# Kernel optimization log

Measured on AMD Instinct MI355X. Metric: run time of the kernel, lower is better.

Reference implementation:

```python
import jax, jax.numpy as jnp
import numpy as np

BS, C, H, W = 4, 128, 64, 64  # input_dim=128
INNER = 64


def setup_inputs() -> dict:
    key = jax.random.key(0)
    ks = jax.random.split(key, 9)
    s_in = 1.0 / np.sqrt(C)
    s_inner = 1.0 / np.sqrt(INNER)
    return {
        "inpt": jax.random.normal(ks[0], (BS, C, H, W), dtype=jnp.float32),
        "Wq": jax.random.normal(ks[1], (INNER, C), dtype=jnp.float32) * s_in,
        "bq": jax.random.normal(ks[2], (INNER,), dtype=jnp.float32) * 0.01,
        "Wk": jax.random.normal(ks[3], (INNER, C), dtype=jnp.float32) * s_in,
        "bk": jax.random.normal(ks[4], (INNER,), dtype=jnp.float32) * 0.01,
        "Wv": jax.random.normal(ks[5], (INNER, C), dtype=jnp.float32) * s_in,
        "bv": jax.random.normal(ks[6], (INNER,), dtype=jnp.float32) * 0.01,
        "Wo": jax.random.normal(ks[7], (C, INNER), dtype=jnp.float32) * s_inner,
        "bo": jax.random.normal(ks[8], (C,), dtype=jnp.float32) * 0.01,
    }


def reference(inpt, Wq, bq, Wk, bk, Wv, bv, Wo, bo):
    bs, c, h, w = inpt.shape
    L = h * w
    # [bs, C, H, W] -> [bs, L, C] (tokens = spatial positions)
    x = inpt.reshape(bs, c, L).transpose(0, 2, 1)
    q = jnp.einsum('blc,dc->bld', x, Wq) + bq  # [bs, L, INNER]
    k = jnp.einsum('blc,dc->bld', x, Wk) + bk
    v = jnp.einsum('blc,dc->bld', x, Wv) + bv
    # torch code divides by np.round(sqrt(d), 2); for d=64 this is exactly 8.0
    scale = jnp.float32(np.round(np.sqrt(q.shape[-1]), 2))
    scores = jnp.einsum('bld,bmd->blm', q, k) / scale  # [bs, L, L] score matrix
    factors = jax.nn.softmax(scores, axis=-1)
    ctx = jnp.einsum('blm,bmd->bld', factors, v)  # [bs, L, INNER]
    out = jnp.einsum('bld,cd->blc', ctx, Wo) + bo  # [bs, L, C]
    out = out.transpose(0, 2, 1).reshape(bs, c, h, w)
    return inpt + out
```

## Files before the change

kernel.cpp:

```cpp
#include <hip/hip_runtime.h>
#include <hip/hip_bf16.h>

typedef __bf16 bf16x8 __attribute__((ext_vector_type(8)));
typedef __bf16 bf16x4 __attribute__((ext_vector_type(4)));
typedef short  s16x4  __attribute__((ext_vector_type(4)));
typedef float  f32x4  __attribute__((ext_vector_type(4)));

#define MFMA32(a, b, c) __builtin_amdgcn_mfma_f32_16x16x32_bf16((a), (b), (c), 0, 0, 0)
#define MFMA16K(a, b, c) __builtin_amdgcn_mfma_f32_16x16x16bf16_1k((a), (b), (c), 0, 0, 0)

#if __has_builtin(__builtin_amdgcn_exp2f)
#define EXP2F(x) __builtin_amdgcn_exp2f(x)
#else
#define EXP2F(x) __expf(0.6931471805599453f * (x))
#endif

#define GL16(G, L)                                                            \
    __builtin_amdgcn_global_load_lds(                                         \
        (const __attribute__((address_space(1))) void*)(G),                   \
        (__attribute__((address_space(3))) void*)(L), 16, 0, 0)

#define SPLIT 4
#define QSCALE 0.18033688011112042f
#define BBOUND 12.0f


__global__ __launch_bounds__(256) void qkv_kernel(
    const float* __restrict__ inpt,
    const float* __restrict__ Wq, const float* __restrict__ bq,
    const float* __restrict__ Wk, const float* __restrict__ bk,
    const float* __restrict__ Wv, const float* __restrict__ bv,
    __bf16* __restrict__ Qws, __bf16* __restrict__ Kws, __bf16* __restrict__ VTws)
{
    __shared__ __align__(16) __bf16 xT[16 * 140];
    __shared__ __align__(16) __bf16 os[16 * 144];
    const int bid = blockIdx.x;
    const int b   = bid >> 8;
    const int l0  = (bid & 255) << 4;
    const int t   = threadIdx.x;

    {
        const int c = t >> 1, half = t & 1;
        const float* xin = inpt + ((size_t)(b * 128 + c)) * 4096 + l0 + half * 8;
        float4 v0 = *(const float4*)xin;
        float4 v1 = *(const float4*)(xin + 4);
        const int tok0 = half * 8;
        xT[(tok0 + 0) * 140 + c] = (__bf16)v0.x;
        xT[(tok0 + 1) * 140 + c] = (__bf16)v0.y;
        xT[(tok0 + 2) * 140 + c] = (__bf16)v0.z;
        xT[(tok0 + 3) * 140 + c] = (__bf16)v0.w;
        xT[(tok0 + 4) * 140 + c] = (__bf16)v1.x;
        xT[(tok0 + 5) * 140 + c] = (__bf16)v1.y;
        xT[(tok0 + 6) * 140 + c] = (__bf16)v1.z;
        xT[(tok0 + 7) * 140 + c] = (__bf16)v1.w;
    }
    __syncthreads();

    const int w    = t >> 6;
    const int lane = t & 63;
    const int quad = lane >> 4;
    const int l15  = lane & 15;

    f32x4 acc[3];
    #pragma unroll
    for (int j = 0; j < 3; ++j)
        #pragma unroll
        for (int r = 0; r < 4; ++r) acc[j][r] = 0.f;

    #pragma unroll
    for (int ks = 0; ks < 4; ++ks) {
        bf16x8 af = *(const bf16x8*)&xT[l15 * 140 + ks * 32 + quad * 8];
        #pragma unroll
        for (int j = 0; j < 3; ++j) {
            const int wn   = w * 3 + j;
            const int msel = wn >> 2;
            const float* W = (msel == 0) ? Wq : ((msel == 1) ? Wk : Wv);
            const float* Wp = W + ((wn & 3) * 16 + l15) * 128 + ks * 32 + quad * 8;
            float4 wa = *(const float4*)Wp;
            float4 wb = *(const float4*)(Wp + 4);
            bf16x8 bf;
            bf[0] = (__bf16)wa.x; bf[1] = (__bf16)wa.y;
            bf[2] = (__bf16)wa.z; bf[3] = (__bf16)wa.w;
            bf[4] = (__bf16)wb.x; bf[5] = (__bf16)wb.y;
            bf[6] = (__bf16)wb.z; bf[7] = (__bf16)wb.w;
            acc[j] = MFMA32(af, bf, acc[j]);
        }
    }

    #pragma unroll
    for (int j = 0; j < 3; ++j) {
        const int wn   = w * 3 + j;
        const int msel = wn >> 2;
        const int o0   = (wn & 3) * 16;
        const float* bb = (msel == 0) ? bq : ((msel == 1) ? bk : bv);
        float bias = bb[o0 + l15];
        if (msel < 2) {
            const float scl = (msel == 0) ? QSCALE : 1.0f;
            const int oc = wn * 16 + l15;
            #pragma unroll
            for (int r = 0; r < 4; ++r)
                os[(quad * 4 + r) * 144 + oc] = (__bf16)((acc[j][r] + bias) * scl);
        } else {
            const int d  = o0 + l15;
            const int kt = l0 >> 6;
            const int kc = (l0 >> 4) & 3;
            bf16x4 v;
            #pragma unroll
            for (int r = 0; r < 4; ++r) v[r] = (__bf16)(acc[j][r] + bias);
            *(bf16x4*)(VTws + (size_t)b * 262144 + kt * 4096
                       + d * 64 + quad * 16 + kc * 4) = v;
        }
    }
    __syncthreads();

    {
        const int tok = t >> 4, c = t & 15;
        bf16x8 v = *(const bf16x8*)&os[tok * 144 + c * 8];
        __bf16* dst = (c < 8)
            ? Qws + ((size_t)(b * 4096 + l0 + tok)) * 64 + c * 8
            : Kws + ((size_t)(b * 4096 + l0 + tok)) * 64 + (c - 8) * 8;
        *(bf16x8*)dst = v;
    }
}

__global__ __launch_bounds__(256, 4) void attn_kernel(
    const __bf16* __restrict__ Qws, const __bf16* __restrict__ Kws,
    const __bf16* __restrict__ VTws,
    float* __restrict__ Ops, float* __restrict__ Lws)
{
    __shared__ __align__(16) __bf16 sbuf[2][8192];

    const int bid   = blockIdx.x;
    const int split = bid >> 8;
    const int qt    = bid & 255;
    const int b  = qt >> 6;
    const int l0 = (qt & 63) << 6;
    const int t    = threadIdx.x;
    const int w    = t >> 6;
    const int lane = t & 63;
    const int quad = lane >> 4;
    const int l15  = lane & 15;

    const __bf16* qptr = Qws + ((size_t)(b * 4096 + l0 + w * 16 + l15)) * 64 + quad * 8;
    bf16x8 qf0 = *(const bf16x8*)qptr;
    bf16x8 qf1 = *(const bf16x8*)(qptr + 32);

    f32x4 cfr[4];
    #pragma unroll
    for (int mt = 0; mt < 4; ++mt)
        #pragma unroll
        for (int r = 0; r < 4; ++r) cfr[mt][r] = 0.f;
    float l_run = 0.f;

    int koff[8], voff[8];
    #pragma unroll
    for (int nt = 0; nt < 4; ++nt) {
        const int key = nt * 16 + l15;
        const int kx  = key & 7;
        koff[nt * 2 + 0] = (key * 8 + (quad ^ kx)) * 8;
        koff[nt * 2 + 1] = (key * 8 + ((quad + 4) ^ kx)) * 8;
    }
    #pragma unroll
    for (int mt = 0; mt < 4; ++mt) {
        const int d = mt * 16 + l15;
        #pragma unroll
        for (int kc8 = 0; kc8 < 2; ++kc8)
            voff[kc8 * 4 + mt] = 4096 + d * 64 + (((2 * quad + kc8) ^ (d & 7)) * 8);
    }

    const uint4* Kg = (const uint4*)(Kws + ((size_t)b << 18));
    const uint4* Vg = (const uint4*)(VTws + ((size_t)b << 18));
    const int rw = t >> 3, cw = (t & 7) ^ ((t >> 3) & 7);
    const uint4* kp = Kg + rw * 8 + cw + split * 8192;
    const uint4* vp = Vg + rw * 8 + cw + split * 8192;

    union B4 { bf16x4 h; s16x4 s; };
    union V8 { bf16x8 v; s16x4 q[2]; };

    auto stage = [&](__bf16* Bb) {
        GL16(kp,       Bb +        w * 512);
        GL16(kp + 256, Bb + 2048 + w * 512);
        GL16(vp,       Bb + 4096 + w * 512);
        GL16(vp + 256, Bb + 6144 + w * 512);
        kp += 512; vp += 512;
    };

    auto tile_step = [&](const __bf16* __restrict__ B) {
        B4 pk[4];
        float ps[4];
        #pragma unroll
        for (int nt = 0; nt < 4; ++nt) {
            bf16x8 kf0 = *(const bf16x8*)&B[koff[nt * 2 + 0]];
            bf16x8 kf1 = *(const bf16x8*)&B[koff[nt * 2 + 1]];
            f32x4 a = {-BBOUND, -BBOUND, -BBOUND, -BBOUND};
            a = MFMA32(kf0, qf0, a);
            a = MFMA32(kf1, qf1, a);
            float p0 = EXP2F(a[0]), p1 = EXP2F(a[1]);
            float p2 = EXP2F(a[2]), p3 = EXP2F(a[3]);
            pk[nt].h[0] = (__bf16)p0; pk[nt].h[1] = (__bf16)p1;
            pk[nt].h[2] = (__bf16)p2; pk[nt].h[3] = (__bf16)p3;
            ps[nt] = (p0 + p1) + (p2 + p3);
        }
        float psum = (ps[0] + ps[1]) + (ps[2] + ps[3]);
        psum += __shfl_xor(psum, 16);
        psum += __shfl_xor(psum, 32);
        l_run += psum;

        #pragma unroll
        for (int kc8 = 0; kc8 < 2; ++kc8) {
            #pragma unroll
            for (int mt = 0; mt < 4; ++mt) {
                V8 vv;
                vv.v = *(const bf16x8*)&B[voff[kc8 * 4 + mt]];
                cfr[mt] = MFMA16K(vv.q[0], pk[2 * kc8 + 0].s, cfr[mt]);
                cfr[mt] = MFMA16K(vv.q[1], pk[2 * kc8 + 1].s, cfr[mt]);
            }
        }
    };

    stage(sbuf[0]);

    __bf16* B0 = sbuf[0];
    __bf16* B1 = sbuf[1];
    for (int kt2 = 0; kt2 < 8; ++kt2) {
        __syncthreads();
        stage(B1);
        tile_step(B0);
        __syncthreads();
        if (kt2 < 7) stage(B0);
        tile_step(B1);
    }

    const int l   = l0 + w * 16 + l15;
    const int row = (split * 4 + b) * 4096 + l;
    float* obase = Ops + (size_t)row * 64;
    #pragma unroll
    for (int mt = 0; mt < 4; ++mt)
        *(f32x4*)(obase + mt * 16 + quad * 4) = cfr[mt];
    if (quad == 0) Lws[row] = l_run;
}

__global__ __launch_bounds__(256) void outproj_kernel(
    const float* __restrict__ inpt,
    const float* __restrict__ Ops, const float* __restrict__ Lws,
    const float* __restrict__ Wo, const float* __restrict__ bo,
    float* __restrict__ out)
{
    __shared__ __align__(16) __bf16 cx[16 * 72];
    const int bid = blockIdx.x;
    const int b   = bid >> 8;
    const int l0  = (bid & 255) << 4;
    const int t   = threadIdx.x;

    {
        const int token = t >> 4, d4 = (t & 15) << 2;
        const int rowb  = b * 4096 + l0 + token;
        float denom = 0.f;
        #pragma unroll
        for (int s = 0; s < SPLIT; ++s) denom += Lws[s * 16384 + rowb];
        const float inv = 1.f / denom;
        float ax = 0.f, ay = 0.f, az = 0.f, aw = 0.f;
        #pragma unroll
        for (int s = 0; s < SPLIT; ++s) {
            const float4 v = *(const float4*)(Ops + ((size_t)(s * 16384 + rowb)) * 64 + d4);
            ax += v.x; ay += v.y; az += v.z; aw += v.w;
        }
        bf16x4 pv;
        pv[0] = (__bf16)(ax * inv); pv[1] = (__bf16)(ay * inv);
        pv[2] = (__bf16)(az * inv); pv[3] = (__bf16)(aw * inv);
        *(bf16x4*)&cx[token * 72 + d4] = pv;
    }
    __syncthreads();

    const int w    = t >> 6;
    const int lane = t & 63;
    const int quad = lane >> 4;
    const int l15  = lane & 15;

    f32x4 acc[2];
    #pragma unroll
    for (int mi = 0; mi < 2; ++mi)
        #pragma unroll
        for (int r = 0; r < 4; ++r) acc[mi][r] = 0.f;

    #pragma unroll
    for (int ks = 0; ks < 2; ++ks) {
        bf16x8 bfrag = *(const bf16x8*)&cx[l15 * 72 + ks * 32 + quad * 8];
        #pragma unroll
        for (int mi = 0; mi < 2; ++mi) {
            const int crow = (w * 2 + mi) * 16 + l15;
            const float* Wp = Wo + crow * 64 + ks * 32 + quad * 8;
            float4 wa = *(const float4*)Wp;
            float4 wb = *(const float4*)(Wp + 4);
            bf16x8 afrag;
            afrag[0] = (__bf16)wa.x; afrag[1] = (__bf16)wa.y;
            afrag[2] = (__bf16)wa.z; afrag[3] = (__bf16)wa.w;
            afrag[4] = (__bf16)wb.x; afrag[5] = (__bf16)wb.y;
            afrag[6] = (__bf16)wb.z; afrag[7] = (__bf16)wb.w;
            acc[mi] = MFMA32(afrag, bfrag, acc[mi]);
        }
    }

    #pragma unroll
    for (int mi = 0; mi < 2; ++mi) {
        #pragma unroll
        for (int r = 0; r < 4; ++r) {
            const int c = (w * 2 + mi) * 16 + quad * 4 + r;
            const size_t addr = ((size_t)(b * 128 + c)) * 4096 + l0 + l15;
            out[addr] = inpt[addr] + bo[c] + acc[mi][r];
        }
    }
}

extern "C" void kernel_launch(void* const* d_in, const int* in_sizes, int n_in,
                              void* d_out, int out_size, void* d_ws, size_t ws_size,
                              hipStream_t stream)
{
    const float* inpt = (const float*)d_in[0];
    const float* Wq   = (const float*)d_in[1];
    const float* bq   = (const float*)d_in[2];
    const float* Wk   = (const float*)d_in[3];
    const float* bk   = (const float*)d_in[4];
    const float* Wv   = (const float*)d_in[5];
    const float* bv   = (const float*)d_in[6];
    const float* Wo   = (const float*)d_in[7];
    const float* bo   = (const float*)d_in[8];
    float* out = (float*)d_out;

    char* ws = (char*)d_ws;
    const size_t MB = (size_t)1 << 20;
    __bf16* Qws  = (__bf16*)(ws + 0 * MB);
    __bf16* Kws  = (__bf16*)(ws + 2 * MB);
    __bf16* VTws = (__bf16*)(ws + 4 * MB);
    float*  Ops  = (float*)(ws + 6 * MB);
    float*  Lws  = (float*)(ws + 23 * MB);

    qkv_kernel<<<1024, 256, 0, stream>>>(inpt, Wq, bq, Wk, bk, Wv, bv, Qws, Kws, VTws);
    attn_kernel<<<SPLIT * 256, 256, 0, stream>>>(Qws, Kws, VTws, Ops, Lws);
    outproj_kernel<<<1024, 256, 0, stream>>>(inpt, Ops, Lws, Wo, bo, out);
}
```

Baseline: 125.9 us.

## Double query rows per wave, split keys eightfold, store partial outputs in bf16

Each wave now handles two 16-row query tiles and reuses every K/V fragment loaded from LDS for both, which halves LDS traffic per unit of MFMA work. The key dimension is split 8 ways instead of 4, so each block walks 512 keys and the grid stays at 1024 blocks. Partial context outputs are written as bf16 instead of fp32, which shrinks the workspace write and the later reduction read. The trade-offs are more registers per thread (two accumulator sets), which may limit occupancy, twice as many partials to combine, and extra rounding from storing unnormalised partials in bf16.

```diff
diff --git a/kernel.cpp b/kernel.cpp
--- a/kernel.cpp
+++ b/kernel.cpp
@@ -20,7 +20,7 @@
         (const __attribute__((address_space(1))) void*)(G),                   \
         (__attribute__((address_space(3))) void*)(L), 16, 0, 0)
 
-#define SPLIT 4
+#define SPLIT 8
 #define QSCALE 0.18033688011112042f
 #define BBOUND 12.0f
 
@@ -126,31 +126,38 @@
 __global__ __launch_bounds__(256, 4) void attn_kernel(
     const __bf16* __restrict__ Qws, const __bf16* __restrict__ Kws,
     const __bf16* __restrict__ VTws,
-    float* __restrict__ Ops, float* __restrict__ Lws)
+    __bf16* __restrict__ Ops, float* __restrict__ Lws)
 {
     __shared__ __align__(16) __bf16 sbuf[2][8192];
 
     const int bid   = blockIdx.x;
-    const int split = bid >> 8;
-    const int qt    = bid & 255;
-    const int b  = qt >> 6;
-    const int l0 = (qt & 63) << 6;
+    const int split = bid >> 7;
+    const int rest  = bid & 127;
+    const int b   = rest >> 5;
+    const int l0  = (rest & 31) << 7;
     const int t    = threadIdx.x;
     const int w    = t >> 6;
     const int lane = t & 63;
     const int quad = lane >> 4;
     const int l15  = lane & 15;
 
-    const __bf16* qptr = Qws + ((size_t)(b * 4096 + l0 + w * 16 + l15)) * 64 + quad * 8;
-    bf16x8 qf0 = *(const bf16x8*)qptr;
-    bf16x8 qf1 = *(const bf16x8*)(qptr + 32);
-
-    f32x4 cfr[4];
-    #pragma unroll
-    for (int mt = 0; mt < 4; ++mt)
-        #pragma unroll
-        for (int r = 0; r < 4; ++r) cfr[mt][r] = 0.f;
-    float l_run = 0.f;
+    bf16x8 qf[2][2];
+    #pragma unroll
+    for (int u = 0; u < 2; ++u) {
+        const __bf16* qptr = Qws
+            + ((size_t)(b * 4096 + l0 + w * 32 + u * 16 + l15)) * 64 + quad * 8;
+        qf[u][0] = *(const bf16x8*)qptr;
+        qf[u][1] = *(const bf16x8*)(qptr + 32);
+    }
+
+    f32x4 cfr[2][4];
+    #pragma unroll
+    for (int u = 0; u < 2; ++u)
+        #pragma unroll
+        for (int mt = 0; mt < 4; ++mt)
+            #pragma unroll
+            for (int r = 0; r < 4; ++r) cfr[u][mt][r] = 0.f;
+    float l_run[2] = {0.f, 0.f};
 
     int koff[8], voff[8];
     #pragma unroll
@@ -171,8 +178,8 @@
     const uint4* Kg = (const uint4*)(Kws + ((size_t)b << 18));
     const uint4* Vg = (const uint4*)(VTws + ((size_t)b << 18));
     const int rw = t >> 3, cw = (t & 7) ^ ((t >> 3) & 7);
-    const uint4* kp = Kg + rw * 8 + cw + split * 8192;
-    const uint4* vp = Vg + rw * 8 + cw + split * 8192;
+    const uint4* kp = Kg + rw * 8 + cw + split * 4096;
+    const uint4* vp = Vg + rw * 8 + cw + split * 4096;
 
     union B4 { bf16x4 h; s16x4 s; };
     union V8 { bf16x8 v; s16x4 q[2]; };
@@ -186,25 +193,31 @@
     };
 
     auto tile_step = [&](const __bf16* __restrict__ B) {
-        B4 pk[4];
-        float ps[4];
+        B4 pk[2][4];
+        float ps[2][4];
         #pragma unroll
         for (int nt = 0; nt < 4; ++nt) {
             bf16x8 kf0 = *(const bf16x8*)&B[koff[nt * 2 + 0]];
             bf16x8 kf1 = *(const bf16x8*)&B[koff[nt * 2 + 1]];
-            f32x4 a = {-BBOUND, -BBOUND, -BBOUND, -BBOUND};
-            a = MFMA32(kf0, qf0, a);
-            a = MFMA32(kf1, qf1, a);
-            float p0 = EXP2F(a[0]), p1 = EXP2F(a[1]);
-            float p2 = EXP2F(a[2]), p3 = EXP2F(a[3]);
-            pk[nt].h[0] = (__bf16)p0; pk[nt].h[1] = (__bf16)p1;
-            pk[nt].h[2] = (__bf16)p2; pk[nt].h[3] = (__bf16)p3;
-            ps[nt] = (p0 + p1) + (p2 + p3);
-        }
-        float psum = (ps[0] + ps[1]) + (ps[2] + ps[3]);
-        psum += __shfl_xor(psum, 16);
-        psum += __shfl_xor(psum, 32);
-        l_run += psum;
+            #pragma unroll
+            for (int u = 0; u < 2; ++u) {
+                f32x4 a = {-BBOUND, -BBOUND, -BBOUND, -BBOUND};
+                a = MFMA32(kf0, qf[u][0], a);
+                a = MFMA32(kf1, qf[u][1], a);
+                float p0 = EXP2F(a[0]), p1 = EXP2F(a[1]);
+                float p2 = EXP2F(a[2]), p3 = EXP2F(a[3]);
+                pk[u][nt].h[0] = (__bf16)p0; pk[u][nt].h[1] = (__bf16)p1;
+                pk[u][nt].h[2] = (__bf16)p2; pk[u][nt].h[3] = (__bf16)p3;
+                ps[u][nt] = (p0 + p1) + (p2 + p3);
+            }
+        }
+        #pragma unroll
+        for (int u = 0; u < 2; ++u) {
+            float psum = (ps[u][0] + ps[u][1]) + (ps[u][2] + ps[u][3]);
+            psum += __shfl_xor(psum, 16);
+            psum += __shfl_xor(psum, 32);
+            l_run[u] += psum;
+        }
 
         #pragma unroll
         for (int kc8 = 0; kc8 < 2; ++kc8) {
@@ -212,8 +225,10 @@
             for (int mt = 0; mt < 4; ++mt) {
                 V8 vv;
                 vv.v = *(const bf16x8*)&B[voff[kc8 * 4 + mt]];
-                cfr[mt] = MFMA16K(vv.q[0], pk[2 * kc8 + 0].s, cfr[mt]);
-                cfr[mt] = MFMA16K(vv.q[1], pk[2 * kc8 + 1].s, cfr[mt]);
+                cfr[0][mt] = MFMA16K(vv.q[0], pk[0][2 * kc8 + 0].s, cfr[0][mt]);
+                cfr[0][mt] = MFMA16K(vv.q[1], pk[0][2 * kc8 + 1].s, cfr[0][mt]);
+                cfr[1][mt] = MFMA16K(vv.q[0], pk[1][2 * kc8 + 0].s, cfr[1][mt]);
+                cfr[1][mt] = MFMA16K(vv.q[1], pk[1][2 * kc8 + 1].s, cfr[1][mt]);
             }
         }
     };
@@ -222,27 +237,34 @@
 
     __bf16* B0 = sbuf[0];
     __bf16* B1 = sbuf[1];
-    for (int kt2 = 0; kt2 < 8; ++kt2) {
+    for (int kt2 = 0; kt2 < 4; ++kt2) {
         __syncthreads();
         stage(B1);
         tile_step(B0);
         __syncthreads();
-        if (kt2 < 7) stage(B0);
+        if (kt2 < 3) stage(B0);
         tile_step(B1);
     }
 
-    const int l   = l0 + w * 16 + l15;
-    const int row = (split * 4 + b) * 4096 + l;
-    float* obase = Ops + (size_t)row * 64;
-    #pragma unroll
-    for (int mt = 0; mt < 4; ++mt)
-        *(f32x4*)(obase + mt * 16 + quad * 4) = cfr[mt];
-    if (quad == 0) Lws[row] = l_run;
+    #pragma unroll
+    for (int u = 0; u < 2; ++u) {
+        const int l   = l0 + w * 32 + u * 16 + l15;
+        const int row = (split * 4 + b) * 4096 + l;
+        __bf16* obase = Ops + (size_t)row * 64;
+        #pragma unroll
+        for (int mt = 0; mt < 4; ++mt) {
+            bf16x4 v;
+            #pragma unroll
+            for (int r = 0; r < 4; ++r) v[r] = (__bf16)cfr[u][mt][r];
+            *(bf16x4*)(obase + mt * 16 + quad * 4) = v;
+        }
+        if (quad == 0) Lws[row] = l_run[u];
+    }
 }
 
 __global__ __launch_bounds__(256) void outproj_kernel(
     const float* __restrict__ inpt,
-    const float* __restrict__ Ops, const float* __restrict__ Lws,
+    const __bf16* __restrict__ Ops, const float* __restrict__ Lws,
     const float* __restrict__ Wo, const float* __restrict__ bo,
     float* __restrict__ out)
 {
@@ -262,8 +284,10 @@
         float ax = 0.f, ay = 0.f, az = 0.f, aw = 0.f;
         #pragma unroll
         for (int s = 0; s < SPLIT; ++s) {
-            const float4 v = *(const float4*)(Ops + ((size_t)(s * 16384 + rowb)) * 64 + d4);
-            ax += v.x; ay += v.y; az += v.z; aw += v.w;
+            const bf16x4 v = *(const bf16x4*)(Ops
+                + ((size_t)(s * 16384 + rowb)) * 64 + d4);
+            ax += (float)v[0]; ay += (float)v[1];
+            az += (float)v[2]; aw += (float)v[3];
         }
         bf16x4 pv;
         pv[0] = (__bf16)(ax * inv); pv[1] = (__bf16)(ay * inv);
@@ -332,10 +356,10 @@
     __bf16* Qws  = (__bf16*)(ws + 0 * MB);
     __bf16* Kws  = (__bf16*)(ws + 2 * MB);
     __bf16* VTws = (__bf16*)(ws + 4 * MB);
-    float*  Ops  = (float*)(ws + 6 * MB);
-    float*  Lws  = (float*)(ws + 23 * MB);
+    __bf16* Ops  = (__bf16*)(ws + 6 * MB);
+    float*  Lws  = (float*)(ws + 24 * MB);
 
     qkv_kernel<<<1024, 256, 0, stream>>>(inpt, Wq, bq, Wk, bk, Wv, bv, Qws, Kws, VTws);
-    attn_kernel<<<SPLIT * 256, 256, 0, stream>>>(Qws, Kws, VTws, Ops, Lws);
+    attn_kernel<<<SPLIT * 128, 256, 0, stream>>>(Qws, Kws, VTws, Ops, Lws);
     outproj_kernel<<<1024, 256, 0, stream>>>(inpt, Ops, Lws, Wo, bo, out);
 }
```

Measured after the change: 152.0 us. 1.21x slower.
